# Kernel tuning notes

Measured on AMD Instinct MI355X. Metric: run time of the kernel, lower is better.

The kernel has to match this reference:

```python
import jax, jax.numpy as jnp
import numpy as np

SCALE = 10.0
KB = 1.0  # kernel_bandwidth

B, D, P, M, K = 128, 128, 4, 100000, 10


def _sqdist(a, b):
    # a: [..., N, D], b: [..., M, D] -> squared euclidean [..., N, M]
    a2 = jnp.sum(a * a, axis=-1)[..., :, None]
    b2 = jnp.sum(b * b, axis=-1)[..., None, :]
    ab = jnp.einsum('...nd,...md->...nm', a, b)
    return jnp.maximum(a2 + b2 - 2.0 * ab, 0.0)


def setup_inputs() -> dict:
    key = jax.random.key(0)
    k1, k2, k3, k4, k5, k6, k7 = jax.random.split(key, 7)
    return {
        'global_img_feat': jax.random.normal(k1, (B, D), jnp.float32),
        'global_text_feat': jax.random.normal(k2, (B, D), jnp.float32),
        'local_img_feats': jax.random.normal(k3, (P, B, D), jnp.float32),
        'centers': jax.random.normal(k4, (P, M, D), jnp.float32),
        'cross_indices': jax.random.randint(k5, (B, K), 0, M, jnp.int64),
        'position': jax.random.randint(k6, (B,), 0, M, jnp.int64),
        'memory_vid': jax.random.randint(k7, (M,), 0, 1000, jnp.int64),
    }


def reference(global_img_feat, global_text_feat, local_img_feats, centers,
              cross_indices, position, memory_vid):
    b = global_img_feat.shape[0]
    # ---- global MMD alignment (text branch detached) ----
    img = global_img_feat / jnp.linalg.norm(global_img_feat, axis=1, keepdims=True)
    txt_d = jax.lax.stop_gradient(global_text_feat)
    txt = txt_d / jnp.linalg.norm(txt_d, axis=1, keepdims=True)
    inv2kb2 = 1.0 / (2.0 * KB * KB)
    k_xx = jnp.exp(-_sqdist(img, img) * inv2kb2)
    k_yy = jnp.exp(-_sqdist(txt, txt) * inv2kb2)
    k_xy = jnp.exp(-_sqdist(img, txt) * inv2kb2)
    off = ~jnp.eye(b, dtype=bool)
    denom = b * (b - 1)
    mmd = (jnp.sum(jnp.where(off, k_xx, 0.0)) / denom
           + jnp.sum(jnp.where(off, k_yy, 0.0)) / denom
           - 2.0 * jnp.mean(k_xy))
    # ---- local part contrastive loss (vectorized over P parts) ----
    m = centers.shape[1]
    pos_feat = centers[:, cross_indices]                       # [P,B,K,D]
    f2 = jnp.sum(local_img_feats ** 2, axis=-1)                # [P,B]
    p2 = jnp.sum(pos_feat ** 2, axis=-1)                       # [P,B,K]
    fp = jnp.einsum('pbd,pbkd->pbk', local_img_feats, pos_feat)
    pos_dist = jnp.sqrt(jnp.maximum(f2[..., None] + p2 - 2.0 * fp, 0.0))  # [P,B,K]
    neg_dist = jnp.sqrt(_sqdist(local_img_feats, centers))     # [P,B,M]
    # negative mask over memory slots (int indices are constants)
    neg_mask = jnp.ones((m,), bool).at[cross_indices.reshape(-1)].set(False)
    neg_mask = neg_mask.at[position].set(False)
    x = jnp.log(jnp.sum(jnp.exp(-SCALE * pos_dist), axis=-1))  # [P,B]
    y = jnp.log(jnp.sum(jnp.exp(-SCALE * neg_dist) * neg_mask[None, None, :], axis=-1))
    l = jnp.sum(-x + y, axis=1) / local_img_feats.shape[1]     # [P]
    l = jnp.where(jnp.isnan(l), 0.0, l)
    local_loss = jnp.sum(l) / local_img_feats.shape[0]
    total = local_loss + 1.0 * mmd
    pos_vid = memory_vid[cross_indices]                        # [B,K]
    return total, local_loss, mmd, pos_vid
```

## Files before the change

kernel.cpp:

```cpp
#include <hip/hip_runtime.h>
#include <math.h>

#define B_ 128
#define D_ 128
#define P_ 4
#define M_ 100000
#define K_ 10
#define SCALE_ 10.0f
#define MB_ 782
#define NEG_BLOCKS (MB_ * P_)
#define MMD_BLOCKS 128
#define POS_BLOCKS 128
#define D2_CUT 120.0f

typedef short bf16x8 __attribute__((ext_vector_type(8)));
typedef float floatx4 __attribute__((ext_vector_type(4)));

__device__ inline unsigned pack_bf16_trunc(unsigned f0, unsigned f1) {
    return __builtin_amdgcn_perm(f1, f0, 0x07060302u);
}

template <int CTRL>
__device__ inline float dpp_add(float v) {
    int x = __builtin_amdgcn_update_dpp(0, __builtin_bit_cast(int, v), CTRL, 0xF, 0xF, true);
    return v + __builtin_bit_cast(float, x);
}
__device__ inline float row16Sum(float v) {
    v = dpp_add<0xB1>(v);
    v = dpp_add<0x4E>(v);
    v = dpp_add<0x141>(v);
    v = dpp_add<0x140>(v);
    return v;
}
__device__ inline float waveSum64(float v) {
    v = row16Sum(v);
    v += __shfl_xor(v, 16, 64);
    v += __shfl_xor(v, 32, 64);
    return v;
}
__device__ inline float waveReduceSumOld(float v) {
    #pragma unroll
    for (int off = 32; off > 0; off >>= 1) v += __shfl_xor(v, off, 64);
    return v;
}
__device__ inline float blockReduce128(float v, float* sh2) {
    v = waveSum64(v);
    int wid = threadIdx.x >> 6;
    if ((threadIdx.x & 63) == 0) sh2[wid] = v;
    __syncthreads();
    float r = sh2[0] + sh2[1];
    __syncthreads();
    return r;
}

__global__ __launch_bounds__(128) void k_prep(const float* __restrict__ img,
                                              const float* __restrict__ txt,
                                              const float* __restrict__ local,
                                              float* imgT, float* txtT,
                                              float* a2i, float* a2t,
                                              float* f2w, float* s_neg,
                                              bf16x8* __restrict__ Apk) {
    __shared__ float sh2[2];
    int bid = blockIdx.x, t = threadIdx.x;
    if (bid < 256) {
        int row = bid & 127, which = bid >> 7;
        if (bid < 4) s_neg[bid * 128 + t] = 0.f;
        const float* src = which ? txt : img;
        float* dstT = which ? txtT : imgT;
        float* a2 = which ? a2t : a2i;
        float v = src[row * D_ + t];
        float s = blockReduce128(v * v, sh2);
        float n = v / sqrtf(s);
        dstT[t * 128 + row] = n;
        float s2 = blockReduce128(n * n, sh2);
        if (t == 0) a2[row] = s2;
    } else if (bid < 768) {
        int r = bid - 256;
        float v = local[(size_t)r * D_ + t];
        float s = blockReduce128(v * v, sh2);
        if (t == 0) f2w[r] = s;
    } else {
        int g = (bid - 768) * 128 + t;
        int p = g >> 11, f = g & 2047;
        int fl = f & 63, bt = (f >> 6) & 7, kc = f >> 9;
        int row = bt * 16 + (fl & 15);
        int col = kc * 32 + ((fl >> 4) & 3) * 8;
        const float* lp = local + (size_t)p * B_ * D_ + row * D_ + col;
        const uint4 u0 = *(const uint4*)lp;
        const uint4 u1 = *(const uint4*)(lp + 4);
        union { bf16x8 v; unsigned u[4]; } fr;
        fr.u[0] = pack_bf16_trunc(u0.x, u0.y);
        fr.u[1] = pack_bf16_trunc(u0.z, u0.w);
        fr.u[2] = pack_bf16_trunc(u1.x, u1.y);
        fr.u[3] = pack_bf16_trunc(u1.z, u1.w);
        Apk[g] = fr.v;
    }
}

__global__ __launch_bounds__(256, 4) void k_main(const float* __restrict__ local,
                                                 const float* __restrict__ centers,
                                                 const float* __restrict__ imgT,
                                                 const float* __restrict__ txtT,
                                                 const float* __restrict__ a2i,
                                                 const float* __restrict__ a2t,
                                                 const int* __restrict__ ci,
                                                 const int* __restrict__ posi,
                                                 const int* __restrict__ mvid,
                                                 const float* __restrict__ f2w,
                                                 const bf16x8* __restrict__ Apk,
                                                 float* __restrict__ s_neg,
                                                 float* __restrict__ s_pos,
                                                 double* __restrict__ mmd_part,
                                                 float* __restrict__ out) {
    union Smem {
        struct {
            bf16x8 A_lds[2048];
            float sred[512];
            float f2l[128];
        } n;
        struct {
            float ri[128], rt[128];
            float sh2[2];
        } m;
    };
    __shared__ Smem sm;
    const int bid = blockIdx.x;
    const int t = threadIdx.x;
    const int w = t >> 6;
    const int l = t & 63;

    if (bid < NEG_BLOCKS) {
        const int p = bid / MB_;
        const int mb = bid - p * MB_;
        const int m0 = mb * 128;
        const int n16 = l & 15;
        const int q = l >> 4;

        int gm[2];
        gm[0] = m0 + (w * 2 + 0) * 16 + n16;
        gm[1] = m0 + (w * 2 + 1) * 16 + n16;
        const float* cb = centers + (size_t)p * M_ * D_;
        uint4 rb[2][4][2];
        if (m0 + 128 <= M_) {
            #pragma unroll
            for (int wm = 0; wm < 2; wm++) {
                const uint4* src = (const uint4*)(cb + (size_t)gm[wm] * D_ + q * 8);
                #pragma unroll
                for (int kc = 0; kc < 4; kc++) {
                    rb[wm][kc][0] = src[kc * 8];
                    rb[wm][kc][1] = src[kc * 8 + 1];
                }
            }
        } else {
            const uint4 z = make_uint4(0u, 0u, 0u, 0u);
            #pragma unroll
            for (int wm = 0; wm < 2; wm++) {
                const uint4* src = (const uint4*)(cb + (size_t)gm[wm] * D_ + q * 8);
                #pragma unroll
                for (int kc = 0; kc < 4; kc++) {
                    if (gm[wm] < M_) {
                        rb[wm][kc][0] = src[kc * 8];
                        rb[wm][kc][1] = src[kc * 8 + 1];
                    } else {
                        rb[wm][kc][0] = z;
                        rb[wm][kc][1] = z;
                    }
                }
            }
        }

        const bf16x8* Ap = Apk + (p << 11);
        #pragma unroll
        for (int s8 = 0; s8 < 8; s8++) {
            int fb = w * 64 + 256 * s8;
            __builtin_amdgcn_global_load_lds(
                (const __attribute__((address_space(1))) void*)(Ap + fb + l),
                (__attribute__((address_space(3))) void*)(&sm.n.A_lds[fb]),
                16, 0, 0);
        }
        if (t < 128) sm.n.f2l[t] = f2w[p * 128 + t];

        float c2a[2];
        bf16x8 bfr[2][4];
        #pragma unroll
        for (int wm = 0; wm < 2; wm++) {
            float c = 0.f;
            #pragma unroll
            for (int kc = 0; kc < 4; kc++) {
                union { uint4 u; floatx4 f; } a, b;
                a.u = rb[wm][kc][0];
                b.u = rb[wm][kc][1];
                c += a.f[0]*a.f[0] + a.f[1]*a.f[1] + a.f[2]*a.f[2] + a.f[3]*a.f[3]
                   + b.f[0]*b.f[0] + b.f[1]*b.f[1] + b.f[2]*b.f[2] + b.f[3]*b.f[3];
                union { bf16x8 v; unsigned u[4]; } fr;
                fr.u[0] = pack_bf16_trunc(a.u.x, a.u.y);
                fr.u[1] = pack_bf16_trunc(a.u.z, a.u.w);
                fr.u[2] = pack_bf16_trunc(b.u.x, b.u.y);
                fr.u[3] = pack_bf16_trunc(b.u.z, b.u.w);
                bfr[wm][kc] = fr.v;
            }
            c2a[wm] = c;
        }

        float c2v[2];
        #pragma unroll
        for (int wm = 0; wm < 2; wm++) {
            float c = c2a[wm];
            c += __shfl_xor(c, 16, 64);
            c += __shfl_xor(c, 32, 64);
            c2v[wm] = c;
        }

        __syncthreads();

        floatx4 acc[8][2];
        #pragma unroll
        for (int bt = 0; bt < 8; bt++) { acc[bt][0] = (floatx4)(0.f); acc[bt][1] = (floatx4)(0.f); }
        #pragma unroll
        for (int kc = 0; kc < 4; kc++) {
            #pragma unroll
            for (int bt = 0; bt < 8; bt++) {
                bf16x8 af = sm.n.A_lds[kc * 512 + bt * 64 + l];
                acc[bt][0] = __builtin_amdgcn_mfma_f32_16x16x32_bf16(af, bfr[0][kc], acc[bt][0], 0, 0, 0);
                acc[bt][1] = __builtin_amdgcn_mfma_f32_16x16x32_bf16(af, bfr[1][kc], acc[bt][1], 0, 0, 0);
            }
        }

        float dmin = 1e30f;
        #pragma unroll
        for (int bt = 0; bt < 8; bt++) {
            floatx4 f4 = *(const floatx4*)&sm.n.f2l[bt * 16 + q * 4];
            #pragma unroll
            for (int r = 0; r < 4; r++) {
                float d20 = fmaf(-2.f, acc[bt][0][r], f4[r] + c2v[0]);
                float d21 = fmaf(-2.f, acc[bt][1][r], f4[r] + c2v[1]);
                dmin = fminf(dmin, fminf(d20, d21));
            }
        }
        if (!__any(dmin < D2_CUT)) {
            sm.n.sred[w * 128 + l] = 0.f;
            sm.n.sred[w * 128 + l + 64] = 0.f;
        } else {
            float vm0 = (gm[0] < M_) ? 1.f : 0.f;
            float vm1 = (gm[1] < M_) ? 1.f : 0.f;
            for (int i = 0; i < B_ * K_; i++) {
                int idx = ci[i];
                if (idx == gm[0]) vm0 = 0.f;
                if (idx == gm[1]) vm1 = 0.f;
            }
            for (int i = 0; i < B_; i++) {
                int idx = posi[i];
                if (idx == gm[0]) vm0 = 0.f;
                if (idx == gm[1]) vm1 = 0.f;
            }
            #pragma unroll
            for (int bt = 0; bt < 8; bt++) {
                floatx4 f4 = *(const floatx4*)&sm.n.f2l[bt * 16 + q * 4];
                #pragma unroll
                for (int r = 0; r < 4; r++) {
                    float s = 0.f;
                    float d20 = fmaxf(fmaf(-2.f, acc[bt][0][r], f4[r] + c2v[0]), 0.f);
                    float d21 = fmaxf(fmaf(-2.f, acc[bt][1][r], f4[r] + c2v[1]), 0.f);
                    if (d20 < D2_CUT) s += vm0 * expf(-SCALE_ * sqrtf(d20));
                    if (d21 < D2_CUT) s += vm1 * expf(-SCALE_ * sqrtf(d21));
                    s = row16Sum(s);
                    if (n16 == 0) sm.n.sred[w * 128 + bt * 16 + q * 4 + r] = s;
                }
            }
        }
        __syncthreads();
        if (t < 128) {
            float s = sm.n.sred[t] + sm.n.sred[128 + t] + sm.n.sred[256 + t] + sm.n.sred[384 + t];
            if (s != 0.f) atomicAdd(&s_neg[p * 128 + t], s);
        }
    } else if (bid < NEG_BLOCKS + MMD_BLOCKS) {
        const int i = bid - NEG_BLOCKS;
        if (t < 128) {
            sm.m.ri[t] = imgT[t * 128 + i];
            sm.m.rt[t] = txtT[t * 128 + i];
        }
        __syncthreads();
        float kxx = 0.f, kyy = 0.f, kxy = 0.f;
        if (t < 128) {
            float dxx = 0.f, dyy = 0.f, dxy = 0.f;
            #pragma unroll 4
            for (int d = 0; d < D_; d++) {
                float rid = sm.m.ri[d], rtd = sm.m.rt[d];
                float av = imgT[d * 128 + t];
                float bv = txtT[d * 128 + t];
                dxx = fmaf(rid, av, dxx);
                dyy = fmaf(rtd, bv, dyy);
                dxy = fmaf(rid, bv, dxy);
            }
            kxx = (i == t) ? 0.f : expf(-fmaxf(a2i[i] + a2i[t] - 2.f * dxx, 0.f) * 0.5f);
            kyy = (i == t) ? 0.f : expf(-fmaxf(a2t[i] + a2t[t] - 2.f * dyy, 0.f) * 0.5f);
            kxy = expf(-fmaxf(a2i[i] + a2t[t] - 2.f * dxy, 0.f) * 0.5f);
        }
        float sxx = waveReduceSumOld(kxx);
        float syy = waveReduceSumOld(kyy);
        float sxy = waveReduceSumOld(kxy);
        __syncthreads();
        if (t == 0)  { sm.m.sh2[0] = sxx; }
        if (t == 64) { sm.m.sh2[1] = sxx; }
        __syncthreads();
        float txx = sm.m.sh2[0] + sm.m.sh2[1];
        __syncthreads();
        if (t == 0)  { sm.m.sh2[0] = syy; }
        if (t == 64) { sm.m.sh2[1] = syy; }
        __syncthreads();
        float tyy = sm.m.sh2[0] + sm.m.sh2[1];
        __syncthreads();
        if (t == 0)  { sm.m.sh2[0] = sxy; }
        if (t == 64) { sm.m.sh2[1] = sxy; }
        __syncthreads();
        float txy = sm.m.sh2[0] + sm.m.sh2[1];
        if (t == 0) {
            mmd_part[i] = (double)txx;
            mmd_part[128 + i] = (double)tyy;
            mmd_part[256 + i] = (double)txy;
        }
    } else {
        const int pair = (bid - (NEG_BLOCKS + MMD_BLOCKS)) * 4 + w;
        const int p = pair >> 7, b = pair & 127;
        const float* f = local + (size_t)pair * D_;
        float f0 = f[l], f1 = f[l + 64];
        float f2v = f2w[pair];
        const float* cb = centers + (size_t)p * M_ * D_;
        float s = 0.f;
        #pragma unroll
        for (int k = 0; k < K_; k++) {
            int idx = ci[b * K_ + k];
            const float* c = cb + (size_t)idx * D_;
            float c0 = c[l], c1 = c[l + 64];
            float p2 = waveSum64(c0 * c0 + c1 * c1);
            float fp = waveSum64(f0 * c0 + f1 * c1);
            float d2 = fmaxf(f2v + p2 - 2.f * fp, 0.f);
            if (d2 < D2_CUT) s += expf(-SCALE_ * sqrtf(d2));
        }
        if (l == 0) s_pos[pair] = s;
        if (p == 0 && l < K_) {
            int ix = ci[b * K_ + l];
            out[3 + b * K_ + l] = (float)mvid[ix];
        }
    }
}

__global__ __launch_bounds__(512) void k_final(const float* __restrict__ s_pos,
                                               const float* __restrict__ s_neg,
                                               const double* __restrict__ mmd_part,
                                               float* out) {
    __shared__ float red[512];
    __shared__ float lp_[4];
    int t = threadIdx.x;
    float x = logf(s_pos[t]);
    float y = logf(s_neg[t]);
    red[t] = -x + y;
    __syncthreads();
    for (int s = 64; s > 0; s >>= 1) {
        if ((t & 127) < s) red[t] += red[t + s];
        __syncthreads();
    }
    if ((t & 127) == 0) {
        float lv = red[t] / (float)B_;
        if (isnan(lv)) lv = 0.f;
        lp_[t >> 7] = lv;
    }
    __syncthreads();
    if (t == 0) {
        float local_loss = (lp_[0] + lp_[1] + lp_[2] + lp_[3]) / (float)P_;
        double sxx = 0.0, syy = 0.0, sxy = 0.0;
        for (int i = 0; i < 128; i++) {
            sxx += mmd_part[i];
            syy += mmd_part[128 + i];
            sxy += mmd_part[256 + i];
        }
        double denom = 128.0 * 127.0;
        float mmd = (float)(sxx / denom + syy / denom - 2.0 * (sxy / (128.0 * 128.0)));
        out[0] = local_loss + mmd;
        out[1] = local_loss;
        out[2] = mmd;
    }
}

extern "C" void kernel_launch(void* const* d_in, const int* in_sizes, int n_in,
                              void* d_out, int out_size, void* d_ws, size_t ws_size,
                              hipStream_t stream) {
    const float* img     = (const float*)d_in[0];
    const float* txt     = (const float*)d_in[1];
    const float* local   = (const float*)d_in[2];
    const float* centers = (const float*)d_in[3];
    const int*   ci      = (const int*)d_in[4];
    const int*   posi    = (const int*)d_in[5];
    const int*   mvid    = (const int*)d_in[6];
    float* out = (float*)d_out;

    char* ws = (char*)d_ws;
    float*  imgT     = (float*)(ws + 0);
    float*  txtT     = (float*)(ws + 65536);
    float*  a2i      = (float*)(ws + 131072);
    float*  a2t      = (float*)(ws + 131584);
    float*  f2w      = (float*)(ws + 132096);
    float*  s_pos    = (float*)(ws + 134144);
    float*  s_neg    = (float*)(ws + 136192);
    double* mmd_part = (double*)(ws + 138240);
    bf16x8* Apk      = (bf16x8*)(ws + 147456);

    k_prep<<<832, 128, 0, stream>>>(img, txt, local, imgT, txtT, a2i, a2t, f2w, s_neg, Apk);
    k_main<<<NEG_BLOCKS + MMD_BLOCKS + POS_BLOCKS, 256, 0, stream>>>(
        local, centers, imgT, txtT, a2i, a2t, ci, posi, mvid, f2w, Apk,
        s_neg, s_pos, mmd_part, out);
    k_final<<<1, 512, 0, stream>>>(s_pos, s_neg, mmd_part, out);
}
```

Baseline: 334.3 us.

## Make negative-distance blocks persistent with register prefetch of next center tile

```diff
diff --git a/kernel.cpp b/kernel.cpp
--- a/kernel.cpp
+++ b/kernel.cpp
@@ -7,8 +7,8 @@
 #define M_ 100000
 #define K_ 10
 #define SCALE_ 10.0f
-#define MB_ 782
-#define NEG_BLOCKS (MB_ * P_)
+#define NTILE 782
+#define NEGB2 512
 #define MMD_BLOCKS 128
 #define POS_BLOCKS 128
 #define D2_CUT 120.0f
@@ -51,6 +51,39 @@
     float r = sh2[0] + sh2[1];
     __syncthreads();
     return r;
+}
+
+__device__ inline void load_tile(uint4 rb[2][4][2], const float* cb, int m0,
+                                 int w, int n16, int q) {
+    if (m0 + 128 <= M_) {
+        #pragma unroll
+        for (int wm = 0; wm < 2; wm++) {
+            const int gmr = m0 + (w * 2 + wm) * 16 + n16;
+            const uint4* src = (const uint4*)(cb + (size_t)gmr * D_ + q * 8);
+            #pragma unroll
+            for (int kc = 0; kc < 4; kc++) {
+                rb[wm][kc][0] = src[kc * 8];
+                rb[wm][kc][1] = src[kc * 8 + 1];
+            }
+        }
+    } else {
+        const uint4 z = make_uint4(0u, 0u, 0u, 0u);
+        #pragma unroll
+        for (int wm = 0; wm < 2; wm++) {
+            const int gmr = m0 + (w * 2 + wm) * 16 + n16;
+            const uint4* src = (const uint4*)(cb + (size_t)gmr * D_ + q * 8);
+            #pragma unroll
+            for (int kc = 0; kc < 4; kc++) {
+                if (gmr < M_) {
+                    rb[wm][kc][0] = src[kc * 8];
+                    rb[wm][kc][1] = src[kc * 8 + 1];
+                } else {
+                    rb[wm][kc][0] = z;
+                    rb[wm][kc][1] = z;
+                }
+            }
+        }
+    }
 }
 
 __global__ __launch_bounds__(128) void k_prep(const float* __restrict__ img,
@@ -97,7 +130,7 @@
     }
 }
 
-__global__ __launch_bounds__(256, 4) void k_main(const float* __restrict__ local,
+__global__ __launch_bounds__(256, 2) void k_main(const float* __restrict__ local,
                                                  const float* __restrict__ centers,
                                                  const float* __restrict__ imgT,
                                                  const float* __restrict__ txtT,
@@ -129,45 +162,12 @@
     const int w = t >> 6;
     const int l = t & 63;
 
-    if (bid < NEG_BLOCKS) {
-        const int p = bid / MB_;
-        const int mb = bid - p * MB_;
-        const int m0 = mb * 128;
+    if (bid < NEGB2) {
+        const int p = bid >> 7;
+        const int g = bid & 127;
         const int n16 = l & 15;
         const int q = l >> 4;
-
-        int gm[2];
-        gm[0] = m0 + (w * 2 + 0) * 16 + n16;
-        gm[1] = m0 + (w * 2 + 1) * 16 + n16;
-        const float* cb = centers + (size_t)p * M_ * D_;
-        uint4 rb[2][4][2];
-        if (m0 + 128 <= M_) {
-            #pragma unroll
-            for (int wm = 0; wm < 2; wm++) {
-                const uint4* src = (const uint4*)(cb + (size_t)gm[wm] * D_ + q * 8);
-                #pragma unroll
-                for (int kc = 0; kc < 4; kc++) {
-                    rb[wm][kc][0] = src[kc * 8];
-                    rb[wm][kc][1] = src[kc * 8 + 1];
-                }
-            }
-        } else {
-            const uint4 z = make_uint4(0u, 0u, 0u, 0u);
-            #pragma unroll
-            for (int wm = 0; wm < 2; wm++) {
-                const uint4* src = (const uint4*)(cb + (size_t)gm[wm] * D_ + q * 8);
-                #pragma unroll
-                for (int kc = 0; kc < 4; kc++) {
-                    if (gm[wm] < M_) {
-                        rb[wm][kc][0] = src[kc * 8];
-                        rb[wm][kc][1] = src[kc * 8 + 1];
-                    } else {
-                        rb[wm][kc][0] = z;
-                        rb[wm][kc][1] = z;
-                    }
-                }
-            }
-        }
+        const int nt = (g < 14) ? 7 : 6;
 
         const bf16x8* Ap = Apk + (p << 11);
         #pragma unroll
@@ -180,92 +180,115 @@
         }
         if (t < 128) sm.n.f2l[t] = f2w[p * 128 + t];
 
-        float c2a[2];
-        bf16x8 bfr[2][4];
-        #pragma unroll
-        for (int wm = 0; wm < 2; wm++) {
-            float c = 0.f;
+        const float* cb = centers + (size_t)p * M_ * D_;
+        int m0 = g * 128;
+
+        float sacc[8][4];
+        #pragma unroll
+        for (int bt = 0; bt < 8; bt++)
+            #pragma unroll
+            for (int r = 0; r < 4; r++) sacc[bt][r] = 0.f;
+
+        uint4 rb[2][4][2];
+        load_tile(rb, cb, m0, w, n16, q);
+
+        __syncthreads();
+
+        for (int ti = 0; ti < nt; ti++) {
+            float c2a[2];
+            bf16x8 bfr[2][4];
+            #pragma unroll
+            for (int wm = 0; wm < 2; wm++) {
+                float c = 0.f;
+                #pragma unroll
+                for (int kc = 0; kc < 4; kc++) {
+                    union { uint4 u; floatx4 f; } a, b;
+                    a.u = rb[wm][kc][0];
+                    b.u = rb[wm][kc][1];
+                    c += a.f[0]*a.f[0] + a.f[1]*a.f[1] + a.f[2]*a.f[2] + a.f[3]*a.f[3]
+                       + b.f[0]*b.f[0] + b.f[1]*b.f[1] + b.f[2]*b.f[2] + b.f[3]*b.f[3];
+                    union { bf16x8 v; unsigned u[4]; } fr;
+                    fr.u[0] = pack_bf16_trunc(a.u.x, a.u.y);
+                    fr.u[1] = pack_bf16_trunc(a.u.z, a.u.w);
+                    fr.u[2] = pack_bf16_trunc(b.u.x, b.u.y);
+                    fr.u[3] = pack_bf16_trunc(b.u.z, b.u.w);
+                    bfr[wm][kc] = fr.v;
+                }
+                c2a[wm] = c;
+            }
+            float c2v[2];
+            #pragma unroll
+            for (int wm = 0; wm < 2; wm++) {
+                float c = c2a[wm];
+                c += __shfl_xor(c, 16, 64);
+                c += __shfl_xor(c, 32, 64);
+                c2v[wm] = c;
+            }
+            const int gm0 = m0 + (w * 2 + 0) * 16 + n16;
+            const int gm1 = m0 + (w * 2 + 1) * 16 + n16;
+
+            if (ti + 1 < nt) load_tile(rb, cb, m0 + 16384, w, n16, q);
+
+            floatx4 acc[8][2];
+            #pragma unroll
+            for (int bt = 0; bt < 8; bt++) { acc[bt][0] = (floatx4)(0.f); acc[bt][1] = (floatx4)(0.f); }
             #pragma unroll
             for (int kc = 0; kc < 4; kc++) {
-                union { uint4 u; floatx4 f; } a, b;
-                a.u = rb[wm][kc][0];
-                b.u = rb[wm][kc][1];
-                c += a.f[0]*a.f[0] + a.f[1]*a.f[1] + a.f[2]*a.f[2] + a.f[3]*a.f[3]
-                   + b.f[0]*b.f[0] + b.f[1]*b.f[1] + b.f[2]*b.f[2] + b.f[3]*b.f[3];
-                union { bf16x8 v; unsigned u[4]; } fr;
-                fr.u[0] = pack_bf16_trunc(a.u.x, a.u.y);
-                fr.u[1] = pack_bf16_trunc(a.u.z, a.u.w);
-                fr.u[2] = pack_bf16_trunc(b.u.x, b.u.y);
-                fr.u[3] = pack_bf16_trunc(b.u.z, b.u.w);
-                bfr[wm][kc] = fr.v;
-            }
-            c2a[wm] = c;
-        }
-
-        float c2v[2];
-        #pragma unroll
-        for (int wm = 0; wm < 2; wm++) {
-            float c = c2a[wm];
-            c += __shfl_xor(c, 16, 64);
-            c += __shfl_xor(c, 32, 64);
-            c2v[wm] = c;
-        }
-
-        __syncthreads();
-
-        floatx4 acc[8][2];
-        #pragma unroll
-        for (int bt = 0; bt < 8; bt++) { acc[bt][0] = (floatx4)(0.f); acc[bt][1] = (floatx4)(0.f); }
-        #pragma unroll
-        for (int kc = 0; kc < 4; kc++) {
-            #pragma unroll
-            for (int bt = 0; bt < 8; bt++) {
-                bf16x8 af = sm.n.A_lds[kc * 512 + bt * 64 + l];
-                acc[bt][0] = __builtin_amdgcn_mfma_f32_16x16x32_bf16(af, bfr[0][kc], acc[bt][0], 0, 0, 0);
-                acc[bt][1] = __builtin_amdgcn_mfma_f32_16x16x32_bf16(af, bfr[1][kc], acc[bt][1], 0, 0, 0);
-            }
-        }
-
-        float dmin = 1e30f;
-        #pragma unroll
-        for (int bt = 0; bt < 8; bt++) {
-            floatx4 f4 = *(const floatx4*)&sm.n.f2l[bt * 16 + q * 4];
-            #pragma unroll
-            for (int r = 0; r < 4; r++) {
-                float d20 = fmaf(-2.f, acc[bt][0][r], f4[r] + c2v[0]);
-                float d21 = fmaf(-2.f, acc[bt][1][r], f4[r] + c2v[1]);
-                dmin = fminf(dmin, fminf(d20, d21));
-            }
-        }
-        if (!__any(dmin < D2_CUT)) {
-            sm.n.sred[w * 128 + l] = 0.f;
-            sm.n.sred[w * 128 + l + 64] = 0.f;
-        } else {
-            float vm0 = (gm[0] < M_) ? 1.f : 0.f;
-            float vm1 = (gm[1] < M_) ? 1.f : 0.f;
-            for (int i = 0; i < B_ * K_; i++) {
-                int idx = ci[i];
-                if (idx == gm[0]) vm0 = 0.f;
-                if (idx == gm[1]) vm1 = 0.f;
-            }
-            for (int i = 0; i < B_; i++) {
-                int idx = posi[i];
-                if (idx == gm[0]) vm0 = 0.f;
-                if (idx == gm[1]) vm1 = 0.f;
-            }
+                #pragma unroll
+                for (int bt = 0; bt < 8; bt++) {
+                    bf16x8 af = sm.n.A_lds[kc * 512 + bt * 64 + l];
+                    acc[bt][0] = __builtin_amdgcn_mfma_f32_16x16x32_bf16(af, bfr[0][kc], acc[bt][0], 0, 0, 0);
+                    acc[bt][1] = __builtin_amdgcn_mfma_f32_16x16x32_bf16(af, bfr[1][kc], acc[bt][1], 0, 0, 0);
+                }
+            }
+
+            float dmin = 1e30f;
             #pragma unroll
             for (int bt = 0; bt < 8; bt++) {
                 floatx4 f4 = *(const floatx4*)&sm.n.f2l[bt * 16 + q * 4];
                 #pragma unroll
                 for (int r = 0; r < 4; r++) {
-                    float s = 0.f;
-                    float d20 = fmaxf(fmaf(-2.f, acc[bt][0][r], f4[r] + c2v[0]), 0.f);
-                    float d21 = fmaxf(fmaf(-2.f, acc[bt][1][r], f4[r] + c2v[1]), 0.f);
-                    if (d20 < D2_CUT) s += vm0 * expf(-SCALE_ * sqrtf(d20));
-                    if (d21 < D2_CUT) s += vm1 * expf(-SCALE_ * sqrtf(d21));
-                    s = row16Sum(s);
-                    if (n16 == 0) sm.n.sred[w * 128 + bt * 16 + q * 4 + r] = s;
-                }
+                    float d20 = fmaf(-2.f, acc[bt][0][r], f4[r] + c2v[0]);
+                    float d21 = fmaf(-2.f, acc[bt][1][r], f4[r] + c2v[1]);
+                    dmin = fminf(dmin, fminf(d20, d21));
+                }
+            }
+            if (__any(dmin < D2_CUT)) {
+                float vm0 = (gm0 < M_) ? 1.f : 0.f;
+                float vm1 = (gm1 < M_) ? 1.f : 0.f;
+                for (int i = 0; i < B_ * K_; i++) {
+                    int idx = ci[i];
+                    if (idx == gm0) vm0 = 0.f;
+                    if (idx == gm1) vm1 = 0.f;
+                }
+                for (int i = 0; i < B_; i++) {
+                    int idx = posi[i];
+                    if (idx == gm0) vm0 = 0.f;
+                    if (idx == gm1) vm1 = 0.f;
+                }
+                #pragma unroll
+                for (int bt = 0; bt < 8; bt++) {
+                    floatx4 f4 = *(const floatx4*)&sm.n.f2l[bt * 16 + q * 4];
+                    #pragma unroll
+                    for (int r = 0; r < 4; r++) {
+                        float d20 = fmaxf(fmaf(-2.f, acc[bt][0][r], f4[r] + c2v[0]), 0.f);
+                        float d21 = fmaxf(fmaf(-2.f, acc[bt][1][r], f4[r] + c2v[1]), 0.f);
+                        float s = 0.f;
+                        if (d20 < D2_CUT) s += vm0 * expf(-SCALE_ * sqrtf(d20));
+                        if (d21 < D2_CUT) s += vm1 * expf(-SCALE_ * sqrtf(d21));
+                        sacc[bt][r] += s;
+                    }
+                }
+            }
+            m0 += 16384;
+        }
+
+        #pragma unroll
+        for (int bt = 0; bt < 8; bt++) {
+            #pragma unroll
+            for (int r = 0; r < 4; r++) {
+                float s = row16Sum(sacc[bt][r]);
+                if (n16 == 0) sm.n.sred[w * 128 + bt * 16 + q * 4 + r] = s;
             }
         }
         __syncthreads();
@@ -273,8 +296,8 @@
             float s = sm.n.sred[t] + sm.n.sred[128 + t] + sm.n.sred[256 + t] + sm.n.sred[384 + t];
             if (s != 0.f) atomicAdd(&s_neg[p * 128 + t], s);
         }
-    } else if (bid < NEG_BLOCKS + MMD_BLOCKS) {
-        const int i = bid - NEG_BLOCKS;
+    } else if (bid < NEGB2 + MMD_BLOCKS) {
+        const int i = bid - NEGB2;
         if (t < 128) {
             sm.m.ri[t] = imgT[t * 128 + i];
             sm.m.rt[t] = txtT[t * 128 + i];
@@ -320,7 +343,7 @@
             mmd_part[256 + i] = (double)txy;
         }
     } else {
-        const int pair = (bid - (NEG_BLOCKS + MMD_BLOCKS)) * 4 + w;
+        const int pair = (bid - (NEGB2 + MMD_BLOCKS)) * 4 + w;
         const int p = pair >> 7, b = pair & 127;
         const float* f = local + (size_t)pair * D_;
         float f0 = f[l], f1 = f[l + 64];
@@ -406,7 +429,7 @@
     bf16x8* Apk      = (bf16x8*)(ws + 147456);
 
     k_prep<<<832, 128, 0, stream>>>(img, txt, local, imgT, txtT, a2i, a2t, f2w, s_neg, Apk);
-    k_main<<<NEG_BLOCKS + MMD_BLOCKS + POS_BLOCKS, 256, 0, stream>>>(
+    k_main<<<NEGB2 + MMD_BLOCKS + POS_BLOCKS, 256, 0, stream>>>(
         local, centers, imgT, txtT, a2i, a2t, ci, posi, mvid, f2w, Apk,
         s_neg, s_pos, mmd_part, out);
     k_final<<<1, 512, 0, stream>>>(s_pos, s_neg, mmd_part, out);
```

Result: slower. 381.0 us (+13.9%).

## Persistent negative-distance blocks with triple-buffered async LDS tile streaming

Applied to the files above, without the earlier changes.

```diff
diff --git a/kernel.cpp b/kernel.cpp
--- a/kernel.cpp
+++ b/kernel.cpp
@@ -7,8 +7,8 @@
 #define M_ 100000
 #define K_ 10
 #define SCALE_ 10.0f
-#define MB_ 782
-#define NEG_BLOCKS (MB_ * P_)
+#define TPP 1563
+#define NEG_BLOCKS 256
 #define MMD_BLOCKS 128
 #define POS_BLOCKS 128
 #define D2_CUT 120.0f
@@ -97,7 +97,7 @@
     }
 }
 
-__global__ __launch_bounds__(256, 4) void k_main(const float* __restrict__ local,
+__global__ __launch_bounds__(256, 2) void k_main(const float* __restrict__ local,
                                                  const float* __restrict__ centers,
                                                  const float* __restrict__ imgT,
                                                  const float* __restrict__ txtT,
@@ -115,6 +115,7 @@
     union Smem {
         struct {
             bf16x8 A_lds[2048];
+            float Bt[3][8192];
             float sred[512];
             float f2l[128];
         } n;
@@ -130,44 +131,13 @@
     const int l = t & 63;
 
     if (bid < NEG_BLOCKS) {
-        const int p = bid / MB_;
-        const int mb = bid - p * MB_;
-        const int m0 = mb * 128;
+        const int p = bid >> 6;
+        const int g = bid & 63;
+        const int nt = (g < 27) ? 25 : 24;
         const int n16 = l & 15;
         const int q = l >> 4;
 
-        int gm[2];
-        gm[0] = m0 + (w * 2 + 0) * 16 + n16;
-        gm[1] = m0 + (w * 2 + 1) * 16 + n16;
-        const float* cb = centers + (size_t)p * M_ * D_;
-        uint4 rb[2][4][2];
-        if (m0 + 128 <= M_) {
-            #pragma unroll
-            for (int wm = 0; wm < 2; wm++) {
-                const uint4* src = (const uint4*)(cb + (size_t)gm[wm] * D_ + q * 8);
-                #pragma unroll
-                for (int kc = 0; kc < 4; kc++) {
-                    rb[wm][kc][0] = src[kc * 8];
-                    rb[wm][kc][1] = src[kc * 8 + 1];
-                }
-            }
-        } else {
-            const uint4 z = make_uint4(0u, 0u, 0u, 0u);
-            #pragma unroll
-            for (int wm = 0; wm < 2; wm++) {
-                const uint4* src = (const uint4*)(cb + (size_t)gm[wm] * D_ + q * 8);
-                #pragma unroll
-                for (int kc = 0; kc < 4; kc++) {
-                    if (gm[wm] < M_) {
-                        rb[wm][kc][0] = src[kc * 8];
-                        rb[wm][kc][1] = src[kc * 8 + 1];
-                    } else {
-                        rb[wm][kc][0] = z;
-                        rb[wm][kc][1] = z;
-                    }
-                }
-            }
-        }
+        if (t < 128) sm.n.f2l[t] = f2w[p * 128 + t];
 
         const bf16x8* Ap = Apk + (p << 11);
         #pragma unroll
@@ -178,94 +148,145 @@
                 (__attribute__((address_space(3))) void*)(&sm.n.A_lds[fb]),
                 16, 0, 0);
         }
-        if (t < 128) sm.n.f2l[t] = f2w[p * 128 + t];
-
-        float c2a[2];
-        bf16x8 bfr[2][4];
+
+        unsigned soff[8];
         #pragma unroll
-        for (int wm = 0; wm < 2; wm++) {
-            float c = 0.f;
+        for (int j = 0; j < 8; j++) {
+            unsigned d = (unsigned)(w * 8 + j) * 1024u + (unsigned)l * 16u;
+            unsigned s = 2u * ((d >> 11) & 3u) + ((d >> 8) & 1u);
+            unsigned e = d ^ (s << 4);
+            unsigned u = e >> 5, hf = (e >> 4) & 1u;
+            soff[j] = (u & 63u) * 512u + (u >> 8) * 128u + ((u >> 6) & 3u) * 32u + hf * 16u;
+        }
+
+        const char* cbp = (const char*)(centers + (size_t)p * M_ * D_);
+        char* BtBase = (char*)&sm.n.Bt[0][0];
+
+        auto DMA_TILE = [&](int m0, int buf) {
+            char* dst = BtBase + buf * 32768 + w * 8192;
+            if (m0 + 64 <= M_) {
+                const char* srcb = cbp + (size_t)m0 * 512;
+                #pragma unroll
+                for (int j = 0; j < 8; j++) {
+                    __builtin_amdgcn_global_load_lds(
+                        (const __attribute__((address_space(1))) void*)(srcb + soff[j]),
+                        (__attribute__((address_space(3))) void*)(dst + j * 1024),
+                        16, 0, 0);
+                }
+            } else {
+                #pragma unroll
+                for (int j = 0; j < 8; j++) {
+                    unsigned d = (unsigned)(w * 8 + j) * 1024u + (unsigned)l * 16u;
+                    unsigned s = 2u * ((d >> 11) & 3u) + ((d >> 8) & 1u);
+                    unsigned e = d ^ (s << 4);
+                    unsigned u = e >> 5, hf = (e >> 4) & 1u;
+                    int row = m0 + (int)(u & 63u);
+                    if (row >= M_) row = M_ - 1;
+                    size_t off = (size_t)row * 512 + (u >> 8) * 128 + ((u >> 6) & 3u) * 32 + hf * 16;
+                    __builtin_amdgcn_global_load_lds(
+                        (const __attribute__((address_space(1))) void*)(cbp + off),
+                        (__attribute__((address_space(3))) void*)(dst + j * 1024),
+                        16, 0, 0);
+                }
+            }
+        };
+
+        float sacc[8][4];
+        #pragma unroll
+        for (int bt = 0; bt < 8; bt++)
+            #pragma unroll
+            for (int r = 0; r < 4; r++) sacc[bt][r] = 0.f;
+
+        int m0 = g * 64;
+        DMA_TILE(m0, 0);
+        if (nt > 1) DMA_TILE(m0 + 4096, 1);
+        int bcur = 0;
+
+        for (int i = 0; i < nt; i++) {
+            if (i < nt - 1) asm volatile("s_waitcnt vmcnt(8)" ::: "memory");
+            else           asm volatile("s_waitcnt vmcnt(0)" ::: "memory");
+            __builtin_amdgcn_s_barrier();
+
+            if (i + 2 < nt) {
+                int b2 = bcur + 2; if (b2 >= 3) b2 -= 3;
+                DMA_TILE(m0 + 8192, b2);
+            }
+
+            const char* bufc = (const char*)(BtBase + bcur * 32768);
+            float c2 = 0.f;
+            bf16x8 bfr[4];
             #pragma unroll
             for (int kc = 0; kc < 4; kc++) {
-                union { uint4 u; floatx4 f; } a, b;
-                a.u = rb[wm][kc][0];
-                b.u = rb[wm][kc][1];
-                c += a.f[0]*a.f[0] + a.f[1]*a.f[1] + a.f[2]*a.f[2] + a.f[3]*a.f[3]
-                   + b.f[0]*b.f[0] + b.f[1]*b.f[1] + b.f[2]*b.f[2] + b.f[3]*b.f[3];
-                union { bf16x8 v; unsigned u[4]; } fr;
-                fr.u[0] = pack_bf16_trunc(a.u.x, a.u.y);
-                fr.u[1] = pack_bf16_trunc(a.u.z, a.u.w);
-                fr.u[2] = pack_bf16_trunc(b.u.x, b.u.y);
-                fr.u[3] = pack_bf16_trunc(b.u.z, b.u.w);
-                bfr[wm][kc] = fr.v;
-            }
-            c2a[wm] = c;
-        }
-
-        float c2v[2];
-        #pragma unroll
-        for (int wm = 0; wm < 2; wm++) {
-            float c = c2a[wm];
-            c += __shfl_xor(c, 16, 64);
-            c += __shfl_xor(c, 32, 64);
-            c2v[wm] = c;
-        }
-
-        __syncthreads();
-
-        floatx4 acc[8][2];
-        #pragma unroll
-        for (int bt = 0; bt < 8; bt++) { acc[bt][0] = (floatx4)(0.f); acc[bt][1] = (floatx4)(0.f); }
-        #pragma unroll
-        for (int kc = 0; kc < 4; kc++) {
-            #pragma unroll
-            for (int bt = 0; bt < 8; bt++) {
-                bf16x8 af = sm.n.A_lds[kc * 512 + bt * 64 + l];
-                acc[bt][0] = __builtin_amdgcn_mfma_f32_16x16x32_bf16(af, bfr[0][kc], acc[bt][0], 0, 0, 0);
-                acc[bt][1] = __builtin_amdgcn_mfma_f32_16x16x32_bf16(af, bfr[1][kc], acc[bt][1], 0, 0, 0);
-            }
-        }
-
-        float dmin = 1e30f;
-        #pragma unroll
-        for (int bt = 0; bt < 8; bt++) {
-            floatx4 f4 = *(const floatx4*)&sm.n.f2l[bt * 16 + q * 4];
-            #pragma unroll
-            for (int r = 0; r < 4; r++) {
-                float d20 = fmaf(-2.f, acc[bt][0][r], f4[r] + c2v[0]);
-                float d21 = fmaf(-2.f, acc[bt][1][r], f4[r] + c2v[1]);
-                dmin = fminf(dmin, fminf(d20, d21));
-            }
-        }
-        if (!__any(dmin < D2_CUT)) {
-            sm.n.sred[w * 128 + l] = 0.f;
-            sm.n.sred[w * 128 + l + 64] = 0.f;
-        } else {
-            float vm0 = (gm[0] < M_) ? 1.f : 0.f;
-            float vm1 = (gm[1] < M_) ? 1.f : 0.f;
-            for (int i = 0; i < B_ * K_; i++) {
-                int idx = ci[i];
-                if (idx == gm[0]) vm0 = 0.f;
-                if (idx == gm[1]) vm1 = 0.f;
-            }
-            for (int i = 0; i < B_; i++) {
-                int idx = posi[i];
-                if (idx == gm[0]) vm0 = 0.f;
-                if (idx == gm[1]) vm1 = 0.f;
-            }
+                unsigned u = (unsigned)((kc * 4 + q) * 64 + (w * 16 + n16));
+                unsigned sb = 2u * (unsigned)q + (unsigned)((n16 >> 3) & 1);
+                unsigned a0 = (u * 32u) ^ (sb << 4);
+                union { floatx4 f; uint4 ui; } h0, h1;
+                h0.f = *(const floatx4*)(bufc + a0);
+                h1.f = *(const floatx4*)(bufc + (a0 ^ 16u));
+                c2 += h0.f[0]*h0.f[0] + h0.f[1]*h0.f[1] + h0.f[2]*h0.f[2] + h0.f[3]*h0.f[3]
+                    + h1.f[0]*h1.f[0] + h1.f[1]*h1.f[1] + h1.f[2]*h1.f[2] + h1.f[3]*h1.f[3];
+                union { bf16x8 v; unsigned uu[4]; } fr;
+                fr.uu[0] = pack_bf16_trunc(h0.ui.x, h0.ui.y);
+                fr.uu[1] = pack_bf16_trunc(h0.ui.z, h0.ui.w);
+                fr.uu[2] = pack_bf16_trunc(h1.ui.x, h1.ui.y);
+                fr.uu[3] = pack_bf16_trunc(h1.ui.z, h1.ui.w);
+                bfr[kc] = fr.v;
+            }
+            c2 += __shfl_xor(c2, 16, 64);
+            c2 += __shfl_xor(c2, 32, 64);
+            const float c2v = c2;
+            const int gm = m0 + w * 16 + n16;
+
+            floatx4 acc[8];
+            #pragma unroll
+            for (int bt = 0; bt < 8; bt++) acc[bt] = (floatx4)(0.f);
+            #pragma unroll
+            for (int kc = 0; kc < 4; kc++) {
+                #pragma unroll
+                for (int bt = 0; bt < 8; bt++) {
+                    bf16x8 af = sm.n.A_lds[kc * 512 + bt * 64 + l];
+                    acc[bt] = __builtin_amdgcn_mfma_f32_16x16x32_bf16(af, bfr[kc], acc[bt], 0, 0, 0);
+                }
+            }
+
+            float dmin = 1e30f;
             #pragma unroll
             for (int bt = 0; bt < 8; bt++) {
                 floatx4 f4 = *(const floatx4*)&sm.n.f2l[bt * 16 + q * 4];
                 #pragma unroll
                 for (int r = 0; r < 4; r++) {
-                    float s = 0.f;
-                    float d20 = fmaxf(fmaf(-2.f, acc[bt][0][r], f4[r] + c2v[0]), 0.f);
-                    float d21 = fmaxf(fmaf(-2.f, acc[bt][1][r], f4[r] + c2v[1]), 0.f);
-                    if (d20 < D2_CUT) s += vm0 * expf(-SCALE_ * sqrtf(d20));
-                    if (d21 < D2_CUT) s += vm1 * expf(-SCALE_ * sqrtf(d21));
-                    s = row16Sum(s);
-                    if (n16 == 0) sm.n.sred[w * 128 + bt * 16 + q * 4 + r] = s;
-                }
+                    float d2 = fmaf(-2.f, acc[bt][r], f4[r] + c2v);
+                    dmin = fminf(dmin, d2);
+                }
+            }
+            if (__any(dmin < D2_CUT)) {
+                float vm = (gm < M_) ? 1.f : 0.f;
+                for (int ii = 0; ii < B_ * K_; ii++) {
+                    if (ci[ii] == gm) vm = 0.f;
+                }
+                for (int ii = 0; ii < B_; ii++) {
+                    if (posi[ii] == gm) vm = 0.f;
+                }
+                #pragma unroll
+                for (int bt = 0; bt < 8; bt++) {
+                    floatx4 f4 = *(const floatx4*)&sm.n.f2l[bt * 16 + q * 4];
+                    #pragma unroll
+                    for (int r = 0; r < 4; r++) {
+                        float d2 = fmaxf(fmaf(-2.f, acc[bt][r], f4[r] + c2v), 0.f);
+                        if (d2 < D2_CUT) sacc[bt][r] += vm * expf(-SCALE_ * sqrtf(d2));
+                    }
+                }
+            }
+            m0 += 4096;
+            bcur = (bcur + 1 == 3) ? 0 : bcur + 1;
+        }
+
+        #pragma unroll
+        for (int bt = 0; bt < 8; bt++) {
+            #pragma unroll
+            for (int r = 0; r < 4; r++) {
+                float s = row16Sum(sacc[bt][r]);
+                if (n16 == 0) sm.n.sred[w * 128 + bt * 16 + q * 4 + r] = s;
             }
         }
         __syncthreads();
```

After: 335.7 us. About the same (+0.4%).
